# Performance work log

Measured on AMD Instinct MI355X. Metric: run time of the kernel, lower is better.

## Reference

```python
import jax, jax.numpy as jnp
import numpy as np

B, T = 2, 1024
V, D, H, L = 32000, 1024, 16, 8
DH = D // H  # 64
ROPE_BASE = 1000.0
EPS = 1e-6


def _rms_norm(x):
    # F.rms_norm(x, (C,), eps=1e-6)
    ms = jnp.mean(jnp.square(x), axis=-1, keepdims=True)
    return x * jax.lax.rsqrt(ms + EPS)


def _rope_tables(t_len):
    quarter = DH // 4
    inv_freq = jnp.concatenate([
        ROPE_BASE ** (-jnp.arange(quarter, dtype=jnp.float32) / quarter),
        jnp.zeros(quarter, dtype=jnp.float32),
    ])  # [DH/2]
    theta = jnp.arange(t_len, dtype=jnp.float32)[:, None] * inv_freq[None, :]  # [T, DH/2]
    return jnp.cos(theta), jnp.sin(theta)


def _apply_rope(x, cos, sin):
    # x: [B, H, T, DH]; cos/sin: [T, DH/2] broadcast to [1,1,T,DH/2]
    half = DH // 2
    x1, x2 = x[..., :half], x[..., half:]
    c = cos[None, None]
    s = sin[None, None]
    return jnp.concatenate([c * x1 - s * x2, s * x1 + c * x2], axis=-1).astype(x.dtype)


def setup_inputs() -> dict:
    key = jax.random.key(0)
    ks = jax.random.split(key, 7)
    s = 0.02
    return {
        "x_indices": jax.random.randint(ks[0], (B, T), 0, V, dtype=jnp.int32),
        "embedding": jax.random.normal(ks[1], (V, D), dtype=jnp.float32) * s,
        "Wqkv": jax.random.normal(ks[2], (L, 3 * D, D), dtype=jnp.float32) * s,
        "Wout": jax.random.normal(ks[3], (L, D, D), dtype=jnp.float32) * s,
        "W1": jax.random.normal(ks[4], (L, 4 * D, D), dtype=jnp.float32) * s,
        "W2": jax.random.normal(ks[5], (L, D, 4 * D), dtype=jnp.float32) * s,
        "lm_head": jax.random.normal(ks[6], (V, D), dtype=jnp.float32) * s,
    }


def reference(x_indices, embedding, Wqkv, Wout, W1, W2, lm_head):
    x = embedding[x_indices]  # [B, T, D]
    cos, sin = _rope_tables(T)
    causal = jnp.tril(jnp.ones((T, T), dtype=bool))  # [T, T]
    neg = jnp.finfo(x.dtype).min
    scale = 1.0 / np.sqrt(DH)

    for l in range(L):
        n = _rms_norm(x)
        qkv = jnp.einsum('btd,ed->bte', n, Wqkv[l])  # [B, T, 3D]
        qkv = qkv.reshape(B, T, 3, H, DH)
        q = jnp.transpose(qkv[:, :, 0], (0, 2, 1, 3))  # [B, H, T, DH]
        k = jnp.transpose(qkv[:, :, 1], (0, 2, 1, 3))
        v = jnp.transpose(qkv[:, :, 2], (0, 2, 1, 3))
        q = _apply_rope(q, cos, sin)
        k = _apply_rope(k, cos, sin)
        scores = jnp.einsum('bhqd,bhkd->bhqk', q, k) * scale
        scores = jnp.where(causal[None, None], scores, neg)
        attn = jax.nn.softmax(scores, axis=-1)
        ctx = jnp.einsum('bhqk,bhkd->bhqd', attn, v)
        ctx = jnp.transpose(ctx, (0, 2, 1, 3)).reshape(B, T, D)
        x = x + jnp.einsum('btd,ed->bte', ctx, Wout[l])
        n = _rms_norm(x)
        h = jnp.square(jax.nn.relu(jnp.einsum('btd,fd->btf', n, W1[l])))  # [B, T, 4D]
        x = x + jnp.einsum('btf,df->btd', h, W2[l])

    logits = jnp.einsum('btd,vd->btv', _rms_norm(x), lm_head)
    return logits.astype(jnp.float32)
```

## Files before the change

kernel.cpp:

```cpp
#include <hip/hip_runtime.h>
#include <hip/hip_bf16.h>
#include <cmath>
#include <cstdint>

#define B_  2
#define T_  1024
#define V_  32000
#define D_  1024
#define H_  16
#define L_  8
#define DH_ 64

typedef __attribute__((ext_vector_type(8))) short bf16x8;
typedef __attribute__((ext_vector_type(4))) float f32x4;

__device__ __forceinline__ ushort f2bf(float f) {
    union { float f; uint32_t u; } v; v.f = f;
    uint32_t r = v.u + 0x7FFFu + ((v.u >> 16) & 1u);
    return (ushort)(r >> 16);
}
__device__ __forceinline__ float bf2f(ushort u) {
    union { uint32_t u; float f; } v; v.u = ((uint32_t)u) << 16;
    return v.f;
}

__device__ __forceinline__ void async_copy16(const void* g, void* l) {
    __builtin_amdgcn_global_load_lds(
        (const __attribute__((address_space(1))) void*)g,
        (__attribute__((address_space(3))) void*)l, 16, 0, 0);
}

__global__ __launch_bounds__(256) void k_cast(const float4* __restrict__ in,
                                              ushort4* __restrict__ out, int n4) {
    for (int i = blockIdx.x * 256 + threadIdx.x; i < n4; i += gridDim.x * 256) {
        float4 v = in[i];
        out[i] = make_ushort4(f2bf(v.x), f2bf(v.y), f2bf(v.z), f2bf(v.w));
    }
}

__global__ void k_rope_tables(float* __restrict__ cosT, float* __restrict__ sinT) {
    int t = blockIdx.x;
    int i = threadIdx.x;
    float invf = (i < 16) ? powf(1000.0f, -(float)i / 16.0f) : 0.0f;
    float th = (float)t * invf;
    cosT[t * 32 + i] = cosf(th);
    sinT[t * 32 + i] = sinf(th);
}

__global__ __launch_bounds__(256) void k_gather(const int* __restrict__ idx,
                                                const float* __restrict__ emb,
                                                float* __restrict__ x) {
    int row = blockIdx.x;
    int id = idx[row];
    const float4* src = (const float4*)(emb + (size_t)id * D_);
    float4* dst = (float4*)(x + (size_t)row * D_);
    dst[threadIdx.x] = src[threadIdx.x];
}

__global__ __launch_bounds__(256) void k_rmsnorm(const float* __restrict__ x,
                                                 ushort* __restrict__ out) {
    int row = blockIdx.x;
    const float4* xr = (const float4*)(x + (size_t)row * D_);
    float4 v = xr[threadIdx.x];
    float ss = v.x * v.x + v.y * v.y + v.z * v.z + v.w * v.w;
    #pragma unroll
    for (int off = 1; off < 64; off <<= 1) ss += __shfl_xor(ss, off);
    __shared__ float wsum[4];
    int lane = threadIdx.x & 63, wv = threadIdx.x >> 6;
    if (lane == 0) wsum[wv] = ss;
    __syncthreads();
    float tot = wsum[0] + wsum[1] + wsum[2] + wsum[3];
    float inv = rsqrtf(tot * (1.0f / D_) + 1e-6f);
    ushort4 r = make_ushort4(f2bf(v.x * inv), f2bf(v.y * inv), f2bf(v.z * inv), f2bf(v.w * inv));
    *(ushort4*)(out + (size_t)row * D_ + threadIdx.x * 4) = r;
}

template<int BN, int EPI, bool OUTBF, bool CONVB>
__global__ __launch_bounds__(256) void k_mfma_gemm(const ushort* __restrict__ A,
                                                   const void* __restrict__ Wp,
                                                   void* __restrict__ Cp,
                                                   const float* __restrict__ Res,
                                                   const float* __restrict__ cosT,
                                                   const float* __restrict__ sinT,
                                                   int M, int N, int K) {
    constexpr int BM = 128;
    constexpr int MI = 4;
    constexpr int NI = BN / 32;
    __shared__ ushort As[2][BM][64];
    __shared__ ushort Bs[2][BN][64];
    const int tid = threadIdx.x;
    const int wid = tid >> 6, lane = tid & 63;
    const int wr = wid >> 1, wc = wid & 1;
    const int r16 = lane & 15, kc = lane >> 4;
    const int rx = (r16 & 7) << 4;
    const int srow8 = tid >> 3;
    const int sdcp = tid & 7;

    const int nwg = gridDim.x * gridDim.y;
    int orig = blockIdx.y * gridDim.x + blockIdx.x;
    int swz = (nwg & 7) ? orig : ((orig & 7) * (nwg >> 3) + (orig >> 3));
    const size_t bm = (size_t)(swz % gridDim.x) * BM;
    const size_t bn = (size_t)(swz / gridDim.x) * BN;

    auto stage = [&](int buf, int k0) {
        #pragma unroll
        for (int i = 0; i < 4; i++) {
            const int row = i * 32 + srow8;
            const ushort* g = A + (bm + row) * (size_t)K + k0 + ((sdcp ^ (row & 7)) * 8);
            async_copy16(g, (char*)As + buf * (BM * 128) + (i * 256 + tid) * 16);
        }
        if constexpr (!CONVB) {
            const ushort* Wb = (const ushort*)Wp;
            #pragma unroll
            for (int i = 0; i < BN / 32; i++) {
                const int row = i * 32 + srow8;
                const ushort* g = Wb + (bn + row) * (size_t)K + k0 + ((sdcp ^ (row & 7)) * 8);
                async_copy16(g, (char*)Bs + buf * (BN * 128) + (i * 256 + tid) * 16);
            }
        } else {
            const float* Wf = (const float*)Wp;
            #pragma unroll
            for (int i = 0; i < BN / 32; i++) {
                const int row = i * 32 + srow8;
                const float* src = Wf + (bn + row) * (size_t)K + k0 + sdcp * 8;
                float4 v0 = *(const float4*)(src);
                float4 v1 = *(const float4*)(src + 4);
                union { ushort u[8]; bf16x8 v; } tmp;
                tmp.u[0] = f2bf(v0.x); tmp.u[1] = f2bf(v0.y);
                tmp.u[2] = f2bf(v0.z); tmp.u[3] = f2bf(v0.w);
                tmp.u[4] = f2bf(v1.x); tmp.u[5] = f2bf(v1.y);
                tmp.u[6] = f2bf(v1.z); tmp.u[7] = f2bf(v1.w);
                *(bf16x8*)((char*)Bs + buf * (BN * 128) + row * 128 + ((sdcp ^ (row & 7)) << 4)) = tmp.v;
            }
        }
    };

    f32x4 acc[MI][NI];
    #pragma unroll
    for (int mi = 0; mi < MI; mi++)
        #pragma unroll
        for (int ni = 0; ni < NI; ni++) {
            f32x4 z = {0.f, 0.f, 0.f, 0.f};
            acc[mi][ni] = z;
        }

    const int KSTEPS = K >> 6;
    stage(0, 0);
    __syncthreads();
    for (int step = 0; step < KSTEPS; ++step) {
        const int cur = step & 1;
        if (step + 1 < KSTEPS) stage(cur ^ 1, (step + 1) << 6);
        #pragma unroll
        for (int kk = 0; kk < 2; kk++) {
            bf16x8 af[MI], bfr[NI];
            #pragma unroll
            for (int mi = 0; mi < MI; mi++)
                af[mi] = *(const bf16x8*)((const char*)As + cur * (BM * 128) +
                                          (wr * 64 + mi * 16 + r16) * 128 +
                                          ((kk * 64 + kc * 16) ^ rx));
            #pragma unroll
            for (int ni = 0; ni < NI; ni++)
                bfr[ni] = *(const bf16x8*)((const char*)Bs + cur * (BN * 128) +
                                           (wc * (BN / 2) + ni * 16 + r16) * 128 +
                                           ((kk * 64 + kc * 16) ^ rx));
            #pragma unroll
            for (int mi = 0; mi < MI; mi++)
                #pragma unroll
                for (int ni = 0; ni < NI; ni++)
                    acc[mi][ni] = __builtin_amdgcn_mfma_f32_16x16x32_bf16(af[mi], bfr[ni],
                                                                          acc[mi][ni], 0, 0, 0);
        }
        __syncthreads();
    }

    #pragma unroll
    for (int mi = 0; mi < MI; mi++) {
        #pragma unroll
        for (int j = 0; j < 4; j++) {
            const size_t row = bm + wr * 64 + mi * 16 + (lane >> 4) * 4 + j;
            if constexpr (EPI == 3) {
                static_assert(BN == 128, "rope epilogue assumes BN=128");
                const int sec = (int)((bn + wc * 64) >> 10);
                if (sec < 2) {
                    const int t = (int)(row & (T_ - 1));
                    #pragma unroll
                    for (int np = 0; np < 2; np++) {
                        const int i1 = np * 16 + r16;
                        float c = cosT[t * 32 + i1], s = sinT[t * 32 + i1];
                        float x1 = acc[mi][np][j], x2 = acc[mi][np + 2][j];
                        acc[mi][np][j]     = c * x1 - s * x2;
                        acc[mi][np + 2][j] = s * x1 + c * x2;
                    }
                }
            }
            #pragma unroll
            for (int ni = 0; ni < NI; ni++) {
                const size_t col = bn + wc * (BN / 2) + ni * 16 + r16;
                float v = acc[mi][ni][j];
                if constexpr (EPI == 1) v += Res[row * N + col];
                if constexpr (EPI == 2) { v = fmaxf(v, 0.f); v *= v; }
                if constexpr (OUTBF) {
                    ((ushort*)Cp)[row * N + col] = f2bf(v);
                } else if constexpr (EPI == 0) {
                    __builtin_nontemporal_store(v, (float*)Cp + row * N + col);
                } else {
                    ((float*)Cp)[row * N + col] = v;
                }
            }
        }
    }
}

__global__ __launch_bounds__(256) void k_attn_mfma(const ushort* __restrict__ qkv,
                                                   ushort* __restrict__ ctx) {
    __shared__ __align__(16) char lds[24576];
    const int tid = threadIdx.x;
    const int w = tid >> 6, lane = tid & 63;
    const int r16 = lane & 15, kc = lane >> 4;
    const int qb = blockIdx.x * 64;
    const int bh = blockIdx.y, b = bh >> 4, h = bh & 15;
    const size_t tok0 = (size_t)b * T_;
    const ushort* qg = qkv + (tok0 + qb) * (3 * D_) + h * DH_;
    const ushort* kg = qkv + tok0 * (3 * D_) + D_ + h * DH_;
    const ushort* vg = qkv + tok0 * (3 * D_) + 2 * D_ + h * DH_;
    const float SCALE_LOG2E = 0.125f * 1.44269504089f;

    #pragma unroll
    for (int i = 0; i < 2; i++) {
        int slot = i * 256 + tid;
        int row = slot >> 3, dcp = slot & 7;
        int d0 = (dcp ^ (row & 7)) * 8;
        async_copy16(qg + (size_t)row * (3 * D_) + d0, lds + 16384 + slot * 16);
    }
    __syncthreads();
    bf16x8 aq[2];
    #pragma unroll
    for (int ks = 0; ks < 2; ks++) {
        int row = w * 16 + r16;
        aq[ks] = *(const bf16x8*)(lds + 16384 + row * 128 + ((ks * 64 + kc * 16) ^ ((row & 7) << 4)));
    }

    f32x4 o[4];
    float m[4], l[4], corr[4];
    #pragma unroll
    for (int nd = 0; nd < 4; nd++) { f32x4 z = {0.f, 0.f, 0.f, 0.f}; o[nd] = z; }
    #pragma unroll
    for (int j = 0; j < 4; j++) { m[j] = -1e30f; l[j] = 0.f; }

    const int nch = (qb >> 6) + 1;
    for (int ch = 0; ch < nch; ch++) {
        const int kb = ch << 6;
        __syncthreads();
        #pragma unroll
        for (int i = 0; i < 2; i++) {
            int slot = i * 256 + tid;
            int row = slot >> 3, dcp = slot & 7;
            int d0 = (dcp ^ (row & 7)) * 8;
            async_copy16(kg + (size_t)(kb + row) * (3 * D_) + d0, lds + slot * 16);
        }
        {
            int key = tid >> 2, dbase = (tid & 3) * 16;
            const ushort* src = vg + (size_t)(kb + key) * (3 * D_) + dbase;
            bf16x8 v0 = *(const bf16x8*)(src);
            bf16x8 v1 = *(const bf16x8*)(src + 8);
            #pragma unroll
            for (int e = 0; e < 8; e++) {
                int d = dbase + e;
                *(ushort*)(lds + 8192 + d * 128 + ((key * 2) ^ ((d & 7) << 4))) = (ushort)v0[e];
                d = dbase + 8 + e;
                *(ushort*)(lds + 8192 + d * 128 + ((key * 2) ^ ((d & 7) << 4))) = (ushort)v1[e];
            }
        }
        __syncthreads();

        f32x4 s[4];
        #pragma unroll
        for (int ni = 0; ni < 4; ni++) { f32x4 z = {0.f, 0.f, 0.f, 0.f}; s[ni] = z; }
        __builtin_amdgcn_s_setprio(1);
        #pragma unroll
        for (int ks = 0; ks < 2; ks++)
            #pragma unroll
            for (int ni = 0; ni < 4; ni++) {
                int row = ni * 16 + r16;
                bf16x8 kf = *(const bf16x8*)(lds + row * 128 + ((ks * 64 + kc * 16) ^ ((row & 7) << 4)));
                s[ni] = __builtin_amdgcn_mfma_f32_16x16x32_bf16(aq[ks], kf, s[ni], 0, 0, 0);
            }
        __builtin_amdgcn_s_setprio(0);

        const bool diag = (kb == qb);
        #pragma unroll
        for (int j = 0; j < 4; j++) {
            const int qrow = qb + w * 16 + kc * 4 + j;
            #pragma unroll
            for (int ni = 0; ni < 4; ni++) {
                float v = s[ni][j] * SCALE_LOG2E;
                if (diag) { int key = kb + ni * 16 + r16; if (key > qrow) v = -1e30f; }
                s[ni][j] = v;
            }
            float t = fmaxf(fmaxf(s[0][j], s[1][j]), fmaxf(s[2][j], s[3][j]));
            #pragma unroll
            for (int off = 1; off < 16; off <<= 1) t = fmaxf(t, __shfl_xor(t, off));
            float mn = fmaxf(m[j], t);
            corr[j] = exp2f(m[j] - mn);
            m[j] = mn;
            float ps = 0.f;
            #pragma unroll
            for (int ni = 0; ni < 4; ni++) {
                float p = exp2f(s[ni][j] - mn);
                s[ni][j] = p;
                ps += p;
            }
            #pragma unroll
            for (int off = 1; off < 16; off <<= 1) ps += __shfl_xor(ps, off);
            l[j] = l[j] * corr[j] + ps;
        }
        #pragma unroll
        for (int ni = 0; ni < 4; ni++)
            #pragma unroll
            for (int j = 0; j < 4; j++) {
                int row = w * 16 + kc * 4 + j;
                *(ushort*)(lds + 16384 + row * 128 + ((ni * 32 + r16 * 2) ^ ((row & 7) << 4))) = f2bf(s[ni][j]);
            }
        #pragma unroll
        for (int nd = 0; nd < 4; nd++)
            #pragma unroll
            for (int j = 0; j < 4; j++) o[nd][j] *= corr[j];
        __builtin_amdgcn_s_setprio(1);
        #pragma unroll
        for (int ks = 0; ks < 2; ks++) {
            int prow = w * 16 + r16;
            bf16x8 pf = *(const bf16x8*)(lds + 16384 + prow * 128 + ((ks * 64 + kc * 16) ^ ((prow & 7) << 4)));
            #pragma unroll
            for (int nd = 0; nd < 4; nd++) {
                int drow = nd * 16 + r16;
                bf16x8 vf = *(const bf16x8*)(lds + 8192 + drow * 128 + ((ks * 64 + kc * 16) ^ ((drow & 7) << 4)));
                o[nd] = __builtin_amdgcn_mfma_f32_16x16x32_bf16(pf, vf, o[nd], 0, 0, 0);
            }
        }
        __builtin_amdgcn_s_setprio(0);
    }

    #pragma unroll
    for (int j = 0; j < 4; j++) {
        float inv = 1.0f / l[j];
        int row = qb + w * 16 + kc * 4 + j;
        ushort* dst = ctx + (tok0 + row) * D_ + h * DH_;
        #pragma unroll
        for (int nd = 0; nd < 4; nd++)
            dst[nd * 16 + r16] = f2bf(o[nd][j] * inv);
    }
}

extern "C" void kernel_launch(void* const* d_in, const int* in_sizes, int n_in,
                              void* d_out, int out_size, void* d_ws, size_t ws_size,
                              hipStream_t stream) {
    const int*   xi   = (const int*)d_in[0];
    const float* emb  = (const float*)d_in[1];
    const float* Wqkv = (const float*)d_in[2];
    const float* Wout = (const float*)d_in[3];
    const float* W1   = (const float*)d_in[4];
    const float* W2   = (const float*)d_in[5];
    const float* lmh  = (const float*)d_in[6];
    float* out = (float*)d_out;

    const size_t NT = (size_t)B_ * T_;
    size_t off = 0;
    auto carve = [&](size_t bytes) -> char* {
        char* r = (char*)d_ws + off;
        off += (bytes + 255) & ~(size_t)255;
        return r;
    };
    float*  xbuf = (float*)carve(NT * D_ * 4);
    ushort* qkv  = (ushort*)carve(NT * 3 * D_ * 2);
    ushort* nb   = (ushort*)carve(NT * D_ * 2);
    ushort* ctxb = (ushort*)carve(NT * D_ * 2);
    ushort* hb   = (ushort*)carve(NT * 4 * D_ * 2);
    float*  cosT = (float*)carve(T_ * 32 * 4);
    float*  sinT = (float*)carve(T_ * 32 * 4);

    const size_t nWqkv = (size_t)L_ * 3 * D_ * D_;
    const size_t nWout = (size_t)L_ * D_ * D_;
    const size_t nW1   = (size_t)L_ * 4 * D_ * D_;
    const size_t nW2   = (size_t)L_ * 4 * D_ * D_;
    const size_t nLmh  = (size_t)V_ * D_;
    ushort* WqkvB = (ushort*)carve(nWqkv * 2);
    ushort* WoutB = (ushort*)carve(nWout * 2);
    ushort* W1B   = (ushort*)carve(nW1 * 2);
    ushort* W2B   = (ushort*)carve(nW2 * 2);
    ushort* lmhB  = (ushort*)carve(nLmh * 2);
    const bool preconv = (off <= ws_size);

    if (preconv) {
        k_cast<<<dim3(2048), dim3(256), 0, stream>>>((const float4*)Wqkv, (ushort4*)WqkvB, (int)(nWqkv / 4));
        k_cast<<<dim3(2048), dim3(256), 0, stream>>>((const float4*)Wout, (ushort4*)WoutB, (int)(nWout / 4));
        k_cast<<<dim3(2048), dim3(256), 0, stream>>>((const float4*)W1,   (ushort4*)W1B,   (int)(nW1 / 4));
        k_cast<<<dim3(2048), dim3(256), 0, stream>>>((const float4*)W2,   (ushort4*)W2B,   (int)(nW2 / 4));
        k_cast<<<dim3(2048), dim3(256), 0, stream>>>((const float4*)lmh,  (ushort4*)lmhB,  (int)(nLmh / 4));
    }

#define LAUNCH_GEMM(BN, EPI, OUTBF, GX, GY, Aq, Wb16, Wf32, Cq, Rq, Mv, Nv, Kv)              \
    do {                                                                                     \
        if (preconv)                                                                         \
            k_mfma_gemm<BN, EPI, OUTBF, false><<<dim3(GX, GY), dim3(256), 0, stream>>>(      \
                (const ushort*)(Aq), (const void*)(Wb16), (void*)(Cq), (Rq), cosT, sinT,     \
                Mv, Nv, Kv);                                                                 \
        else                                                                                 \
            k_mfma_gemm<BN, EPI, OUTBF, true><<<dim3(GX, GY), dim3(256), 0, stream>>>(       \
                (const ushort*)(Aq), (const void*)(Wf32), (void*)(Cq), (Rq), cosT, sinT,     \
                Mv, Nv, Kv);                                                                 \
    } while (0)

    k_rope_tables<<<dim3(T_), dim3(32), 0, stream>>>(cosT, sinT);
    k_gather<<<dim3(NT), dim3(256), 0, stream>>>(xi, emb, xbuf);

    for (int l = 0; l < L_; l++) {
        k_rmsnorm<<<dim3(NT), dim3(256), 0, stream>>>(xbuf, nb);
        LAUNCH_GEMM(128, 3, true, 16, 24, nb,
                    WqkvB + (size_t)l * 3 * D_ * D_, Wqkv + (size_t)l * 3 * D_ * D_,
                    qkv, nullptr, (int)NT, 3 * D_, D_);
        k_attn_mfma<<<dim3(T_ / 64, B_ * H_), dim3(256), 0, stream>>>(qkv, ctxb);
        LAUNCH_GEMM(64, 1, false, 16, 16, ctxb,
                    WoutB + (size_t)l * D_ * D_, Wout + (size_t)l * D_ * D_,
                    xbuf, xbuf, (int)NT, D_, D_);
        k_rmsnorm<<<dim3(NT), dim3(256), 0, stream>>>(xbuf, nb);
        LAUNCH_GEMM(128, 2, true, 16, 32, nb,
                    W1B + (size_t)l * 4 * D_ * D_, W1 + (size_t)l * 4 * D_ * D_,
                    hb, nullptr, (int)NT, 4 * D_, D_);
        LAUNCH_GEMM(64, 1, false, 16, 16, hb,
                    W2B + (size_t)l * 4 * D_ * D_, W2 + (size_t)l * 4 * D_ * D_,
                    xbuf, xbuf, (int)NT, D_, 4 * D_);
    }
    k_rmsnorm<<<dim3(NT), dim3(256), 0, stream>>>(xbuf, nb);
    LAUNCH_GEMM(128, 0, false, 16, 250, nb, lmhB, lmh, out, nullptr, (int)NT, V_, D_);
#undef LAUNCH_GEMM
}
```

Measured before the change: 1.986 ms.

## Widen attention key chunks to 128 and use a wider single-buffered lm_head tile

```diff
diff --git a/kernel.cpp b/kernel.cpp
--- a/kernel.cpp
+++ b/kernel.cpp
@@ -76,18 +76,20 @@
 }
 
 template<int BN, int EPI, bool OUTBF, bool CONVB>
-__global__ __launch_bounds__(256) void k_mfma_gemm(const ushort* __restrict__ A,
-                                                   const void* __restrict__ Wp,
-                                                   void* __restrict__ Cp,
-                                                   const float* __restrict__ Res,
-                                                   const float* __restrict__ cosT,
-                                                   const float* __restrict__ sinT,
-                                                   int M, int N, int K) {
+__global__ __launch_bounds__(256, 2) void k_mfma_gemm(const ushort* __restrict__ A,
+                                                      const void* __restrict__ Wp,
+                                                      void* __restrict__ Cp,
+                                                      const float* __restrict__ Res,
+                                                      const float* __restrict__ cosT,
+                                                      const float* __restrict__ sinT,
+                                                      int M, int N, int K) {
     constexpr int BM = 128;
     constexpr int MI = 4;
     constexpr int NI = BN / 32;
-    __shared__ ushort As[2][BM][64];
-    __shared__ ushort Bs[2][BN][64];
+    constexpr bool DBUF = (BN <= 128);
+    constexpr int NB = DBUF ? 2 : 1;
+    __shared__ ushort As[NB][BM][64];
+    __shared__ ushort Bs[NB][BN][64];
     const int tid = threadIdx.x;
     const int wid = tid >> 6, lane = tid & 63;
     const int wr = wid >> 1, wc = wid & 1;
@@ -144,23 +146,18 @@
             acc[mi][ni] = z;
         }
 
-    const int KSTEPS = K >> 6;
-    stage(0, 0);
-    __syncthreads();
-    for (int step = 0; step < KSTEPS; ++step) {
-        const int cur = step & 1;
-        if (step + 1 < KSTEPS) stage(cur ^ 1, (step + 1) << 6);
+    auto compute = [&](int buf) {
         #pragma unroll
         for (int kk = 0; kk < 2; kk++) {
             bf16x8 af[MI], bfr[NI];
             #pragma unroll
             for (int mi = 0; mi < MI; mi++)
-                af[mi] = *(const bf16x8*)((const char*)As + cur * (BM * 128) +
+                af[mi] = *(const bf16x8*)((const char*)As + buf * (BM * 128) +
                                           (wr * 64 + mi * 16 + r16) * 128 +
                                           ((kk * 64 + kc * 16) ^ rx));
             #pragma unroll
             for (int ni = 0; ni < NI; ni++)
-                bfr[ni] = *(const bf16x8*)((const char*)Bs + cur * (BN * 128) +
+                bfr[ni] = *(const bf16x8*)((const char*)Bs + buf * (BN * 128) +
                                            (wc * (BN / 2) + ni * 16 + r16) * 128 +
                                            ((kk * 64 + kc * 16) ^ rx));
             #pragma unroll
@@ -170,7 +167,25 @@
                     acc[mi][ni] = __builtin_amdgcn_mfma_f32_16x16x32_bf16(af[mi], bfr[ni],
                                                                           acc[mi][ni], 0, 0, 0);
         }
+    };
+
+    const int KSTEPS = K >> 6;
+    if constexpr (DBUF) {
+        stage(0, 0);
         __syncthreads();
+        for (int step = 0; step < KSTEPS; ++step) {
+            const int cur = step & 1;
+            if (step + 1 < KSTEPS) stage(cur ^ 1, (step + 1) << 6);
+            compute(cur);
+            __syncthreads();
+        }
+    } else {
+        for (int step = 0; step < KSTEPS; ++step) {
+            stage(0, step << 6);
+            __syncthreads();
+            compute(0);
+            __syncthreads();
+        }
     }
 
     #pragma unroll
@@ -213,10 +228,11 @@
 
 __global__ __launch_bounds__(256) void k_attn_mfma(const ushort* __restrict__ qkv,
                                                    ushort* __restrict__ ctx) {
-    __shared__ __align__(16) char lds[24576];
+    __shared__ __align__(16) char lds[49152];
     const int tid = threadIdx.x;
     const int w = tid >> 6, lane = tid & 63;
     const int r16 = lane & 15, kc = lane >> 4;
+    const int rx = (r16 & 7) << 4;
     const int qb = blockIdx.x * 64;
     const int bh = blockIdx.y, b = bh >> 4, h = bh & 15;
     const size_t tok0 = (size_t)b * T_;
@@ -230,14 +246,14 @@
         int slot = i * 256 + tid;
         int row = slot >> 3, dcp = slot & 7;
         int d0 = (dcp ^ (row & 7)) * 8;
-        async_copy16(qg + (size_t)row * (3 * D_) + d0, lds + 16384 + slot * 16);
+        async_copy16(qg + (size_t)row * (3 * D_) + d0, lds + 32768 + slot * 16);
     }
     __syncthreads();
     bf16x8 aq[2];
     #pragma unroll
     for (int ks = 0; ks < 2; ks++) {
         int row = w * 16 + r16;
-        aq[ks] = *(const bf16x8*)(lds + 16384 + row * 128 + ((ks * 64 + kc * 16) ^ ((row & 7) << 4)));
+        aq[ks] = *(const bf16x8*)(lds + 32768 + row * 128 + ((ks * 64 + kc * 16) ^ rx));
     }
 
     f32x4 o[4];
@@ -247,57 +263,60 @@
     #pragma unroll
     for (int j = 0; j < 4; j++) { m[j] = -1e30f; l[j] = 0.f; }
 
-    const int nch = (qb >> 6) + 1;
+    const int nch = (qb >> 7) + 1;
     for (int ch = 0; ch < nch; ch++) {
-        const int kb = ch << 6;
+        const int kb = ch << 7;
         __syncthreads();
         #pragma unroll
-        for (int i = 0; i < 2; i++) {
+        for (int i = 0; i < 4; i++) {
             int slot = i * 256 + tid;
             int row = slot >> 3, dcp = slot & 7;
             int d0 = (dcp ^ (row & 7)) * 8;
             async_copy16(kg + (size_t)(kb + row) * (3 * D_) + d0, lds + slot * 16);
         }
-        {
-            int key = tid >> 2, dbase = (tid & 3) * 16;
+        #pragma unroll
+        for (int r = 0; r < 2; r++) {
+            int key = r * 64 + (tid >> 2), dbase = (tid & 3) * 16;
             const ushort* src = vg + (size_t)(kb + key) * (3 * D_) + dbase;
             bf16x8 v0 = *(const bf16x8*)(src);
             bf16x8 v1 = *(const bf16x8*)(src + 8);
             #pragma unroll
             for (int e = 0; e < 8; e++) {
                 int d = dbase + e;
-                *(ushort*)(lds + 8192 + d * 128 + ((key * 2) ^ ((d & 7) << 4))) = (ushort)v0[e];
+                *(ushort*)(lds + 16384 + d * 256 + ((key * 2) ^ ((d & 7) << 4))) = (ushort)v0[e];
                 d = dbase + 8 + e;
-                *(ushort*)(lds + 8192 + d * 128 + ((key * 2) ^ ((d & 7) << 4))) = (ushort)v1[e];
+                *(ushort*)(lds + 16384 + d * 256 + ((key * 2) ^ ((d & 7) << 4))) = (ushort)v1[e];
             }
         }
         __syncthreads();
 
-        f32x4 s[4];
-        #pragma unroll
-        for (int ni = 0; ni < 4; ni++) { f32x4 z = {0.f, 0.f, 0.f, 0.f}; s[ni] = z; }
+        f32x4 s[8];
+        #pragma unroll
+        for (int ni = 0; ni < 8; ni++) { f32x4 z = {0.f, 0.f, 0.f, 0.f}; s[ni] = z; }
         __builtin_amdgcn_s_setprio(1);
         #pragma unroll
         for (int ks = 0; ks < 2; ks++)
             #pragma unroll
-            for (int ni = 0; ni < 4; ni++) {
+            for (int ni = 0; ni < 8; ni++) {
                 int row = ni * 16 + r16;
-                bf16x8 kf = *(const bf16x8*)(lds + row * 128 + ((ks * 64 + kc * 16) ^ ((row & 7) << 4)));
+                bf16x8 kf = *(const bf16x8*)(lds + row * 128 + ((ks * 64 + kc * 16) ^ rx));
                 s[ni] = __builtin_amdgcn_mfma_f32_16x16x32_bf16(aq[ks], kf, s[ni], 0, 0, 0);
             }
         __builtin_amdgcn_s_setprio(0);
 
-        const bool diag = (kb == qb);
+        const bool diag = (ch == nch - 1);
         #pragma unroll
         for (int j = 0; j < 4; j++) {
             const int qrow = qb + w * 16 + kc * 4 + j;
             #pragma unroll
-            for (int ni = 0; ni < 4; ni++) {
+            for (int ni = 0; ni < 8; ni++) {
                 float v = s[ni][j] * SCALE_LOG2E;
                 if (diag) { int key = kb + ni * 16 + r16; if (key > qrow) v = -1e30f; }
                 s[ni][j] = v;
             }
-            float t = fmaxf(fmaxf(s[0][j], s[1][j]), fmaxf(s[2][j], s[3][j]));
+            float t0 = fmaxf(fmaxf(s[0][j], s[1][j]), fmaxf(s[2][j], s[3][j]));
+            float t1 = fmaxf(fmaxf(s[4][j], s[5][j]), fmaxf(s[6][j], s[7][j]));
+            float t = fmaxf(t0, t1);
             #pragma unroll
             for (int off = 1; off < 16; off <<= 1) t = fmaxf(t, __shfl_xor(t, off));
             float mn = fmaxf(m[j], t);
@@ -305,7 +324,7 @@
             m[j] = mn;
             float ps = 0.f;
             #pragma unroll
-            for (int ni = 0; ni < 4; ni++) {
+            for (int ni = 0; ni < 8; ni++) {
                 float p = exp2f(s[ni][j] - mn);
                 s[ni][j] = p;
                 ps += p;
@@ -315,11 +334,11 @@
             l[j] = l[j] * corr[j] + ps;
         }
         #pragma unroll
-        for (int ni = 0; ni < 4; ni++)
+        for (int ni = 0; ni < 8; ni++)
             #pragma unroll
             for (int j = 0; j < 4; j++) {
                 int row = w * 16 + kc * 4 + j;
-                *(ushort*)(lds + 16384 + row * 128 + ((ni * 32 + r16 * 2) ^ ((row & 7) << 4))) = f2bf(s[ni][j]);
+                *(ushort*)(lds + 32768 + row * 256 + ((ni * 32 + r16 * 2) ^ ((row & 7) << 4))) = f2bf(s[ni][j]);
             }
         #pragma unroll
         for (int nd = 0; nd < 4; nd++)
@@ -327,13 +346,13 @@
             for (int j = 0; j < 4; j++) o[nd][j] *= corr[j];
         __builtin_amdgcn_s_setprio(1);
         #pragma unroll
-        for (int ks = 0; ks < 2; ks++) {
+        for (int ks = 0; ks < 4; ks++) {
             int prow = w * 16 + r16;
-            bf16x8 pf = *(const bf16x8*)(lds + 16384 + prow * 128 + ((ks * 64 + kc * 16) ^ ((prow & 7) << 4)));
+            bf16x8 pf = *(const bf16x8*)(lds + 32768 + prow * 256 + ((ks * 64 + kc * 16) ^ rx));
             #pragma unroll
             for (int nd = 0; nd < 4; nd++) {
                 int drow = nd * 16 + r16;
-                bf16x8 vf = *(const bf16x8*)(lds + 8192 + drow * 128 + ((ks * 64 + kc * 16) ^ ((drow & 7) << 4)));
+                bf16x8 vf = *(const bf16x8*)(lds + 16384 + drow * 256 + ((ks * 64 + kc * 16) ^ rx));
                 o[nd] = __builtin_amdgcn_mfma_f32_16x16x32_bf16(pf, vf, o[nd], 0, 0, 0);
             }
         }
@@ -431,6 +450,6 @@
                     xbuf, xbuf, (int)NT, D_, 4 * D_);
     }
     k_rmsnorm<<<dim3(NT), dim3(256), 0, stream>>>(xbuf, nb);
-    LAUNCH_GEMM(128, 0, false, 16, 250, nb, lmhB, lmh, out, nullptr, (int)NT, V_, D_);
+    LAUNCH_GEMM(256, 0, false, 16, 125, nb, lmhB, lmh, out, nullptr, (int)NT, V_, D_);
 #undef LAUNCH_GEMM
 }
```

After: 1.884 ms. 5.1% less time.
